# Kernel optimization log

Hardware: AMD Instinct MI355X
Metric: run time of the kernel (lower is better)

## Reference

```python
import jax, jax.numpy as jnp
import numpy as np

N = 50000
E = 800000
IN_C = 64
OUT_C = 64
EPS = 1 + 1e-06


def setup_inputs() -> dict:
    key = jax.random.key(0)
    ks = jax.random.split(key, 10)
    x = jax.random.normal(ks[0], (N, IN_C), dtype=jnp.float32)
    lower_indices = jax.random.randint(ks[1], (2, E), 0, N, dtype=jnp.int64)
    lower_values = jax.random.uniform(ks[2], (E,), dtype=jnp.float32)
    upper_indices = jax.random.randint(ks[3], (2, E), 0, N, dtype=jnp.int64)
    upper_values = jax.random.uniform(ks[4], (E,), dtype=jnp.float32)
    s = 1.0 / np.sqrt(IN_C)
    w_lower = jax.random.uniform(ks[5], (IN_C, OUT_C), jnp.float32, -s, s)
    a_lower = jax.random.uniform(ks[6], (2 * OUT_C,), jnp.float32, -s, s)
    w_upper = jax.random.uniform(ks[7], (IN_C, OUT_C), jnp.float32, -s, s)
    a_upper = jax.random.uniform(ks[8], (2 * OUT_C,), jnp.float32, -s, s)
    w_lin = jax.random.uniform(ks[9], (IN_C, OUT_C), jnp.float32, -s, s)
    return {
        "x": x,
        "lower_indices": lower_indices,
        "lower_values": lower_values,
        "upper_indices": upper_indices,
        "upper_values": upper_values,
        "w_lower": w_lower,
        "a_lower": a_lower,
        "w_upper": w_upper,
        "a_upper": a_upper,
        "w_lin": w_lin,
    }


def _att_conv(x, weight, att_w, indices, values):
    """TopoModelX base Conv with att=True.

    x_msg = x @ weight; per edge (i=target, j=source):
      alpha_e = elu(concat(x_msg[j], x_msg[i]) @ att_w) * nbhd_vals_e
    out[i] = sum_e alpha_e * x_msg[j]
    """
    xm = x @ weight                              # [N, out]
    i, j = indices[0], indices[1]                # target, source
    # concat(src, tgt) @ a == src @ a[:F] + tgt @ a[F:]; precompute per-node
    s_src = xm @ att_w[:OUT_C]                   # [N]
    s_tgt = xm @ att_w[OUT_C:]                   # [N]
    alpha = jax.nn.elu(s_src[j] + s_tgt[i]) * values   # [E]
    msg = alpha[:, None] * xm[j]                 # [E, out]
    return jax.ops.segment_sum(msg, i, num_segments=N)


def reference(x, lower_indices, lower_values, upper_indices, upper_values,
              w_lower, a_lower, w_upper, a_upper, w_lin):
    lower_x = _att_conv(x, w_lower, a_lower, lower_indices, lower_values)
    upper_x = _att_conv(x, w_upper, a_upper, upper_indices, upper_values)
    w_x = (x @ w_lin) * EPS
    # Aggregation(aggr_func='sum', update_func='relu')
    return jax.nn.relu(lower_x + upper_x + w_x)
```

## Files before the change

### kernel.cpp

```cpp
#include <hip/hip_runtime.h>
#include <hip/hip_bf16.h>
#include <math.h>

#define N_NODES 50000
#define N_EDGES 800000
#define C 64
#define EPS_F 1.000001f

#define CAPN 48
#define NCNT (2 * N_NODES)
#define OVF_IDX NCNT
#define OMAX 4096

#define RB_BITS 7
#define RBUK (1 << RB_BITS)
#define NREG ((NCNT + RBUK - 1) >> RB_BITS)
#define RCAP 2560
#define EPB 8192
#define NP1 ((2 * N_EDGES + EPB - 1) / EPB)
#define NPREB 784
#define NK1 (NP1 + NPREB)

#define ZERON (NCNT + 1 + NREG)

#define RANGE 16
#define NGATH (N_NODES / RANGE)
#define LDS_STRIDE 66

#define NPRE ((N_NODES + 31) / 32)

typedef __attribute__((ext_vector_type(8))) unsigned short u16x8;

__device__ __forceinline__ unsigned short f2bf(float f) {
    unsigned u = __float_as_uint(f);
    return (unsigned short)((u + 0x7FFFu + ((u >> 16) & 1u)) >> 16);
}
__device__ __forceinline__ float bf2f(unsigned short b) {
    return __uint_as_float(((unsigned)b) << 16);
}

__global__ __launch_bounds__(256) void s_kernel(
    const float* __restrict__ x,
    const float* __restrict__ w_l, const float* __restrict__ a_l,
    const float* __restrict__ w_u, const float* __restrict__ a_u,
    float* __restrict__ ssl, float* __restrict__ stl,
    float* __restrict__ ssu, float* __restrict__ stu,
    int* __restrict__ cnt)
{
    const int b = blockIdx.x;
    const int t = threadIdx.x;

    const int gz = b * 256 + t;
    if (gz < ZERON) cnt[gz] = 0;

    __shared__ float wa[4 * C];
    {
        const int v = t >> 6;
        const int k = t & 63;
        const float* __restrict__ w = (v < 2) ? w_l : w_u;
        const float* __restrict__ a = (v < 2) ? a_l : a_u;
        const int ao = (v & 1) * C;
        float acc = 0.f;
#pragma unroll 16
        for (int o = 0; o < C; ++o)
            acc = fmaf(w[k * C + o], a[ao + o], acc);
        wa[v * C + k] = acc;
    }
    __syncthreads();

    const int lane = t & 63;
    const int wv = t >> 6;
    const int row0 = b * 32 + wv * 8;
    if (row0 >= N_NODES) return;

    const float wls = wa[lane], wlt = wa[C + lane];
    const float wus = wa[2 * C + lane], wut = wa[3 * C + lane];

#pragma unroll
    for (int r = 0; r < 8; ++r) {
        const int row = row0 + r;
        if (row >= N_NODES) break;
        const float xv = x[row * C + lane];
        float psl = xv * wls, ptl = xv * wlt;
        float psu = xv * wus, ptu = xv * wut;
#pragma unroll
        for (int o = 32; o >= 1; o >>= 1) {
            psl += __shfl_xor(psl, o);
            ptl += __shfl_xor(ptl, o);
            psu += __shfl_xor(psu, o);
            ptu += __shfl_xor(ptu, o);
        }
        if (lane == 0) {
            ssl[row] = psl; stl[row] = ptl;
            ssu[row] = psu; stu[row] = ptu;
        }
    }
}

__global__ __launch_bounds__(512) void gemm_scatter_kernel(
    const float* __restrict__ x,
    const float* __restrict__ w_l, const float* __restrict__ w_u,
    const float* __restrict__ w_lin,
    const int* __restrict__ lidx, const float* __restrict__ lval,
    const int* __restrict__ uidx, const float* __restrict__ uval,
    const float* __restrict__ ssl, const float* __restrict__ stl,
    const float* __restrict__ ssu, const float* __restrict__ stu,
    unsigned short* __restrict__ xm_l, unsigned short* __restrict__ xm_u,
    float* __restrict__ xlin,
    int* __restrict__ cnt, uint2* __restrict__ rbuf, int2* __restrict__ ovf)
{
    const int b = blockIdx.x, t = threadIdx.x;
    __shared__ int hist[NREG];

    if (b % 5 == 0) {
        const int p = b / 5;
        int* __restrict__ rcur = cnt + NCNT + 1;

        for (int s0 = t; s0 < NREG; s0 += 512) hist[s0] = 0;
        __syncthreads();

        unsigned lo[16];
        int bk[16];
        const int gbase = p * EPB + t;
#pragma unroll
        for (int k = 0; k < 16; ++k) {
            const int g = gbase + k * 512;
            bk[k] = -1;
            if (g < 2 * N_EDGES) {
                int i, j;
                float v, s;
                if (g < N_EDGES) {
                    i = lidx[g]; j = lidx[N_EDGES + g]; v = lval[g];
                    s = ssl[j] + stl[i];
                    bk[k] = i;
                } else {
                    const int e = g - N_EDGES;
                    i = uidx[e]; j = uidx[N_EDGES + e]; v = uval[e];
                    s = ssu[j] + stu[i];
                    bk[k] = N_NODES + i;
                }
                s = (s > 0.f) ? s : expm1f(s);
                lo[k] = ((unsigned)j << 16) | (unsigned)f2bf(s * v);
                atomicAdd(&hist[bk[k] >> RB_BITS], 1);
            }
        }
        __syncthreads();

        for (int cb = t; cb < NREG; cb += 512) {
            const int c = hist[cb];
            hist[cb] = c ? atomicAdd(&rcur[cb], c) : 0;
        }
        __syncthreads();

#pragma unroll
        for (int k = 0; k < 16; ++k) {
            if (bk[k] >= 0) {
                const int cb = bk[k] >> RB_BITS;
                const int slot = atomicAdd(&hist[cb], 1);
                if (slot < RCAP) {
                    rbuf[(size_t)cb * RCAP + slot] = make_uint2(lo[k], (unsigned)bk[k]);
                } else {
                    const int oi = atomicAdd(&cnt[OVF_IDX], 1);
                    if (oi < OMAX) ovf[oi] = make_int2(bk[k], (int)lo[k]);
                }
            }
        }
        return;
    }

    const int pid = b - b / 5 - 1;
    const int lane = t & 63;
    const int wvu = __builtin_amdgcn_readfirstlane(t >> 6);
    const int row0 = pid * 64 + wvu * 8;
    if (row0 >= N_NODES) return;

    const float* xr[8];
#pragma unroll
    for (int r = 0; r < 8; ++r) {
        int rr = row0 + r;
        if (rr >= N_NODES) rr = N_NODES - 1;
        xr[r] = x + (size_t)rr * C;
    }

    float acc_l[8] = {0,0,0,0,0,0,0,0};
    float acc_u[8] = {0,0,0,0,0,0,0,0};
    float acc_n[8] = {0,0,0,0,0,0,0,0};

#pragma unroll 1
    for (int kc = 0; kc < C; kc += 4) {
#pragma unroll
        for (int kk = 0; kk < 4; ++kk) {
            const int k = kc + kk;
            const float wl = w_l[k * C + lane];
            const float wu = w_u[k * C + lane];
            const float wn = w_lin[k * C + lane];
#pragma unroll
            for (int r = 0; r < 8; ++r) {
                const float xk = xr[r][k];
                acc_l[r] = fmaf(xk, wl, acc_l[r]);
                acc_u[r] = fmaf(xk, wu, acc_u[r]);
                acc_n[r] = fmaf(xk, wn, acc_n[r]);
            }
        }
    }

#pragma unroll
    for (int r = 0; r < 8; ++r) {
        const int row = row0 + r;
        if (row < N_NODES) {
            xm_l[row * C + lane] = f2bf(acc_l[r]);
            xm_u[row * C + lane] = f2bf(acc_u[r]);
            xlin[row * C + lane] = acc_n[r] * EPS_F;
        }
    }
}

__global__ __launch_bounds__(256) void distrib_kernel(
    int* __restrict__ cnt, const uint2* __restrict__ rbuf,
    unsigned* __restrict__ rec, int2* __restrict__ ovf)
{
    const int cb = blockIdx.x, t = threadIdx.x;
    __shared__ int cur[RBUK];
    if (t < RBUK) cur[t] = 0;
    __syncthreads();

    const int* __restrict__ rcur = cnt + NCNT + 1;
    const int n = min(rcur[cb], RCAP);
    const uint2* __restrict__ rb = rbuf + (size_t)cb * RCAP;

    for (int r = t; r < n; r += 256) {
        const uint2 e = rb[r];
        const int local = (int)e.y & (RBUK - 1);
        const int rank = atomicAdd(&cur[local], 1);
        if (rank < CAPN) {
            rec[(size_t)e.y * CAPN + rank] = e.x;
        } else {
            const int oi = atomicAdd(&cnt[OVF_IDX], 1);
            if (oi < OMAX) ovf[oi] = make_int2((int)e.y, (int)e.x);
        }
    }
    __syncthreads();

    if (t < RBUK) {
        const int bucket = (cb << RB_BITS) + t;
        if (bucket < NCNT) cnt[bucket] = cur[t];
    }
}

__global__ __launch_bounds__(256) void gather_kernel(
    const float* __restrict__ xlin,
    const int* __restrict__ cnt, const unsigned* __restrict__ rec,
    const int2* __restrict__ ovf,
    const unsigned short* __restrict__ xm_l, const unsigned short* __restrict__ xm_u,
    float* __restrict__ out)
{
    const int r = blockIdx.x;
    const int t = threadIdx.x;
    const int wv = t >> 6, lane = t & 63;
    const int sub8 = lane >> 3;
    const int cg = lane & 7;

    __shared__ float racc[RANGE * LDS_STRIDE];

    const int oc = min(cnt[OVF_IDX], OMAX);

#pragma unroll 1
    for (int nsel = 0; nsel < 4; ++nsel) {
        const int node = r * RANGE + wv * 4 + nsel;
        const int bA = node;
        const int bB = N_NODES + node;
        const int lenA = min(cnt[bA], CAPN);
        const int lenB = min(cnt[bB], CAPN);
        const unsigned* __restrict__ rbA = rec + (size_t)bA * CAPN;
        const unsigned* __restrict__ rbB = rec + (size_t)bB * CAPN;

        float acc[8] = {0.f,0.f,0.f,0.f,0.f,0.f,0.f,0.f};
        int kA = 0, kB = 0;
        while ((kA < lenA) | (kB < lenB)) {
            const int iA = kA + sub8, iB = kB + sub8;
            const bool aA = iA < lenA, aB = iB < lenB;
            const unsigned rwA = rbA[aA ? iA : kA];
            const unsigned rwB = rbB[aB ? iB : kB];
            const int jA = aA ? (int)(rwA >> 16) : 0;
            const int jB = aB ? (int)(rwB >> 16) : 0;
            const float wA = aA ? bf2f((unsigned short)(rwA & 0xFFFFu)) : 0.f;
            const float wB = aB ? bf2f((unsigned short)(rwB & 0xFFFFu)) : 0.f;
            const u16x8 rowA = *(const u16x8*)(xm_l + jA * C + cg * 8);
            const u16x8 rowB = *(const u16x8*)(xm_u + jB * C + cg * 8);
#pragma unroll
            for (int c = 0; c < 8; ++c)
                acc[c] = fmaf(wA, bf2f(rowA[c]), acc[c]);
#pragma unroll
            for (int c = 0; c < 8; ++c)
                acc[c] = fmaf(wB, bf2f(rowB[c]), acc[c]);
            kA += (kA < lenA) ? 8 : 0;
            kB += (kB < lenB) ? 8 : 0;
        }

        for (int u = 0; u < oc; ++u) {
            const int2 e = ovf[u];
            if (e.x == bA || e.x == bB) {
                const unsigned rw = (unsigned)e.y;
                const int j = (int)(rw >> 16);
                const float w = (sub8 == 0) ? bf2f((unsigned short)(rw & 0xFFFFu)) : 0.f;
                const unsigned short* xm = (e.x == bA) ? xm_l : xm_u;
                const u16x8 row = *(const u16x8*)(xm + j * C + cg * 8);
#pragma unroll
                for (int c = 0; c < 8; ++c)
                    acc[c] = fmaf(w, bf2f(row[c]), acc[c]);
            }
        }

#pragma unroll
        for (int o = 8; o <= 32; o <<= 1)
#pragma unroll
            for (int c = 0; c < 8; ++c)
                acc[c] += __shfl_xor(acc[c], o);
        const int nl = wv * 4 + nsel;
        if (lane < 8) {
#pragma unroll
            for (int c = 0; c < 8; ++c)
                racc[nl * LDS_STRIDE + lane * 8 + c] = acc[c];
        }
    }
    __syncthreads();

    const int base_node = r * RANGE;
#pragma unroll
    for (int rep = 0; rep < 4; ++rep) {
        const int flat = rep * 256 + t;
        const int nl = flat >> 6, ch = flat & 63;
        const int node = base_node + nl;
        const float v = racc[nl * LDS_STRIDE + ch] + xlin[node * C + ch];
        out[node * C + ch] = fmaxf(v, 0.f);
    }
}

extern "C" void kernel_launch(void* const* d_in, const int* in_sizes, int n_in,
                              void* d_out, int out_size, void* d_ws, size_t ws_size,
                              hipStream_t stream)
{
    const float* x          = (const float*)d_in[0];
    const int*   lower_idx  = (const int*)d_in[1];
    const float* lower_vals = (const float*)d_in[2];
    const int*   upper_idx  = (const int*)d_in[3];
    const float* upper_vals = (const float*)d_in[4];
    const float* w_lower    = (const float*)d_in[5];
    const float* a_lower    = (const float*)d_in[6];
    const float* w_upper    = (const float*)d_in[7];
    const float* a_upper    = (const float*)d_in[8];
    const float* w_lin      = (const float*)d_in[9];

    float* out = (float*)d_out;
    char* ws = (char*)d_ws;

    const size_t NC_F = (size_t)N_NODES * C * sizeof(float);
    const size_t NC_H = (size_t)N_NODES * C * sizeof(unsigned short);
    unsigned short* xm_l = (unsigned short*)ws;  ws += NC_H;
    unsigned short* xm_u = (unsigned short*)ws;  ws += NC_H;
    float* xlin = (float*)ws;                 ws += NC_F;
    float* ssl  = (float*)ws;                 ws += N_NODES * sizeof(float);
    float* stl  = (float*)ws;                 ws += N_NODES * sizeof(float);
    float* ssu  = (float*)ws;                 ws += N_NODES * sizeof(float);
    float* stu  = (float*)ws;                 ws += N_NODES * sizeof(float);
    int2* ovf   = (int2*)ws;                  ws += OMAX * sizeof(int2);
    uint2* rbuf = (uint2*)ws;                 ws += (size_t)NREG * RCAP * sizeof(uint2);
    int* cnt    = (int*)ws;                   ws += (size_t)(ZERON + 32) * sizeof(int);
    unsigned* rec = (unsigned*)ws;            ws += ((size_t)NCNT * CAPN + 64) * sizeof(unsigned);

    s_kernel<<<NPRE, 256, 0, stream>>>(
        x, w_lower, a_lower, w_upper, a_upper,
        ssl, stl, ssu, stu, cnt);

    gemm_scatter_kernel<<<NK1, 512, 0, stream>>>(
        x, w_lower, w_upper, w_lin,
        lower_idx, lower_vals, upper_idx, upper_vals,
        ssl, stl, ssu, stu,
        xm_l, xm_u, xlin, cnt, rbuf, ovf);

    distrib_kernel<<<NREG, 256, 0, stream>>>(cnt, rbuf, rec, ovf);

    gather_kernel<<<NGATH, 256, 0, stream>>>(
        xlin, cnt, rec, ovf, xm_l, xm_u, out);
}
```

Measured before the change: 200.2 us.

## Fuse bucket distribution into gather using LDS lists and interleaved buckets

Bucket IDs are interleaved (2*i for lower, 2*i+1 for upper) so that each coarse region of 128 buckets covers 64 nodes. The distrib kernel is removed. The gather kernel now builds per-node edge lists in shared memory straight from the region buffer and then aggregates, which drops the global rec array write and read plus one kernel launch. Per-block overflow goes to a small LDS list. The new block uses about 25KB of LDS and 512 threads, which may lower occupancy.

```diff
diff --git a/kernel.cpp b/kernel.cpp
--- a/kernel.cpp
+++ b/kernel.cpp
@@ -8,24 +8,21 @@
 #define EPS_F 1.000001f
 
 #define CAPN 48
-#define NCNT (2 * N_NODES)
-#define OVF_IDX NCNT
+#define OVF_IDX 0
 #define OMAX 4096
+#define LOVF 64
 
 #define RB_BITS 7
 #define RBUK (1 << RB_BITS)
-#define NREG ((NCNT + RBUK - 1) >> RB_BITS)
+#define NBUCK (2 * N_NODES)
+#define NREG ((NBUCK + RBUK - 1) >> RB_BITS)
 #define RCAP 2560
 #define EPB 8192
 #define NP1 ((2 * N_EDGES + EPB - 1) / EPB)
 #define NPREB 784
 #define NK1 (NP1 + NPREB)
 
-#define ZERON (NCNT + 1 + NREG)
-
-#define RANGE 16
-#define NGATH (N_NODES / RANGE)
-#define LDS_STRIDE 66
+#define ZERON (1 + NREG)
 
 #define NPRE ((N_NODES + 31) / 32)
 
@@ -114,7 +111,7 @@
 
     if (b % 5 == 0) {
         const int p = b / 5;
-        int* __restrict__ rcur = cnt + NCNT + 1;
+        int* __restrict__ rcur = cnt + 1;
 
         for (int s0 = t; s0 < NREG; s0 += 512) hist[s0] = 0;
         __syncthreads();
@@ -132,12 +129,12 @@
                 if (g < N_EDGES) {
                     i = lidx[g]; j = lidx[N_EDGES + g]; v = lval[g];
                     s = ssl[j] + stl[i];
-                    bk[k] = i;
+                    bk[k] = 2 * i;
                 } else {
                     const int e = g - N_EDGES;
                     i = uidx[e]; j = uidx[N_EDGES + e]; v = uval[e];
                     s = ssu[j] + stu[i];
-                    bk[k] = N_NODES + i;
+                    bk[k] = 2 * i + 1;
                 }
                 s = (s > 0.f) ? s : expm1f(s);
                 lo[k] = ((unsigned)j << 16) | (unsigned)f2bf(s * v);
@@ -215,72 +212,65 @@
     }
 }
 
-__global__ __launch_bounds__(256) void distrib_kernel(
-    int* __restrict__ cnt, const uint2* __restrict__ rbuf,
-    unsigned* __restrict__ rec, int2* __restrict__ ovf)
+__global__ __launch_bounds__(512) void gather_kernel(
+    const float* __restrict__ xlin,
+    const int* __restrict__ cnt, const uint2* __restrict__ rbuf,
+    const int2* __restrict__ ovf,
+    const unsigned short* __restrict__ xm_l, const unsigned short* __restrict__ xm_u,
+    float* __restrict__ out)
 {
-    const int cb = blockIdx.x, t = threadIdx.x;
+    const int cb = blockIdx.x;
+    const int t = threadIdx.x;
+    const int wv = t >> 6, lane = t & 63;
+    const int sub8 = lane >> 3;
+    const int cg = lane & 7;
+
+    __shared__ unsigned lists[RBUK * CAPN];
     __shared__ int cur[RBUK];
-    if (t < RBUK) cur[t] = 0;
+    __shared__ int lovf_bk[LOVF];
+    __shared__ unsigned lovf_rc[LOVF];
+    __shared__ int lc;
+
+    for (int s0 = t; s0 < RBUK; s0 += 512) cur[s0] = 0;
+    if (t == 0) lc = 0;
     __syncthreads();
 
-    const int* __restrict__ rcur = cnt + NCNT + 1;
-    const int n = min(rcur[cb], RCAP);
+    const int n = min(cnt[1 + cb], RCAP);
     const uint2* __restrict__ rb = rbuf + (size_t)cb * RCAP;
-
-    for (int r = t; r < n; r += 256) {
+    for (int r = t; r < n; r += 512) {
         const uint2 e = rb[r];
         const int local = (int)e.y & (RBUK - 1);
         const int rank = atomicAdd(&cur[local], 1);
         if (rank < CAPN) {
-            rec[(size_t)e.y * CAPN + rank] = e.x;
+            lists[local * CAPN + rank] = e.x;
         } else {
-            const int oi = atomicAdd(&cnt[OVF_IDX], 1);
-            if (oi < OMAX) ovf[oi] = make_int2((int)e.y, (int)e.x);
+            const int o = atomicAdd(&lc, 1);
+            if (o < LOVF) { lovf_bk[o] = local; lovf_rc[o] = e.x; }
         }
     }
     __syncthreads();
 
-    if (t < RBUK) {
-        const int bucket = (cb << RB_BITS) + t;
-        if (bucket < NCNT) cnt[bucket] = cur[t];
-    }
-}
-
-__global__ __launch_bounds__(256) void gather_kernel(
-    const float* __restrict__ xlin,
-    const int* __restrict__ cnt, const unsigned* __restrict__ rec,
-    const int2* __restrict__ ovf,
-    const unsigned short* __restrict__ xm_l, const unsigned short* __restrict__ xm_u,
-    float* __restrict__ out)
-{
-    const int r = blockIdx.x;
-    const int t = threadIdx.x;
-    const int wv = t >> 6, lane = t & 63;
-    const int sub8 = lane >> 3;
-    const int cg = lane & 7;
-
-    __shared__ float racc[RANGE * LDS_STRIDE];
-
     const int oc = min(cnt[OVF_IDX], OMAX);
+    const int lc2 = min(lc, LOVF);
 
 #pragma unroll 1
-    for (int nsel = 0; nsel < 4; ++nsel) {
-        const int node = r * RANGE + wv * 4 + nsel;
-        const int bA = node;
-        const int bB = N_NODES + node;
-        const int lenA = min(cnt[bA], CAPN);
-        const int lenB = min(cnt[bB], CAPN);
-        const unsigned* __restrict__ rbA = rec + (size_t)bA * CAPN;
-        const unsigned* __restrict__ rbB = rec + (size_t)bB * CAPN;
+    for (int p = 0; p < 8; ++p) {
+        const int q = wv * 8 + p;
+        const int node = cb * 64 + q;
+        if (node >= N_NODES) break;
+        const int lA = 2 * q, lB = 2 * q + 1;
+        const int lenA = min(cur[lA], CAPN);
+        const int lenB = min(cur[lB], CAPN);
+        const unsigned* __restrict__ lstA = lists + lA * CAPN;
+        const unsigned* __restrict__ lstB = lists + lB * CAPN;
 
         float acc[8] = {0.f,0.f,0.f,0.f,0.f,0.f,0.f,0.f};
         int kA = 0, kB = 0;
         while ((kA < lenA) | (kB < lenB)) {
             const int iA = kA + sub8, iB = kB + sub8;
             const bool aA = iA < lenA, aB = iB < lenB;
-            const unsigned rwA = rbA[aA ? iA : kA];
-            const unsigned rwB = rbB[aB ? iB : kB];
+            const unsigned rwA = lstA[aA ? iA : kA];
+            const unsigned rwB = lstB[aB ? iB : kB];
             const int jA = aA ? (int)(rwA >> 16) : 0;
             const int jB = aB ? (int)(rwB >> 16) : 0;
             const float wA = aA ? bf2f((unsigned short)(rwA & 0xFFFFu)) : 0.f;
@@ -299,11 +289,11 @@
 
         for (int u = 0; u < oc; ++u) {
             const int2 e = ovf[u];
-            if (e.x == bA || e.x == bB) {
+            if (e.x == 2 * node || e.x == 2 * node + 1) {
                 const unsigned rw = (unsigned)e.y;
                 const int j = (int)(rw >> 16);
                 const float w = (sub8 == 0) ? bf2f((unsigned short)(rw & 0xFFFFu)) : 0.f;
-                const unsigned short* xm = (e.x == bA) ? xm_l : xm_u;
+                const unsigned short* xm = (e.x & 1) ? xm_u : xm_l;
                 const u16x8 row = *(const u16x8*)(xm + j * C + cg * 8);
 #pragma unroll
                 for (int c = 0; c < 8; ++c)
@@ -311,28 +301,43 @@
             }
         }
 
+        for (int u = 0; u < lc2; ++u) {
+            const int bkl = lovf_bk[u];
+            if (bkl == lA || bkl == lB) {
+                const unsigned rw = lovf_rc[u];
+                const int j = (int)(rw >> 16);
+                const float w = (sub8 == 0) ? bf2f((unsigned short)(rw & 0xFFFFu)) : 0.f;
+                const unsigned short* xm = (bkl & 1) ? xm_u : xm_l;
+                const u16x8 row = *(const u16x8*)(xm + j * C + cg * 8);
+#pragma unroll
+                for (int c = 0; c < 8; ++c)
+                    acc[c] = fmaf(w, bf2f(row[c]), acc[c]);
+            }
+        }
+
 #pragma unroll
         for (int o = 8; o <= 32; o <<= 1)
 #pragma unroll
             for (int c = 0; c < 8; ++c)
                 acc[c] += __shfl_xor(acc[c], o);
-        const int nl = wv * 4 + nsel;
+
         if (lane < 8) {
-#pragma unroll
-            for (int c = 0; c < 8; ++c)
-                racc[nl * LDS_STRIDE + lane * 8 + c] = acc[c];
-        }
-    }
-    __syncthreads();
-
-    const int base_node = r * RANGE;
-#pragma unroll
-    for (int rep = 0; rep < 4; ++rep) {
-        const int flat = rep * 256 + t;
-        const int nl = flat >> 6, ch = flat & 63;
-        const int node = base_node + nl;
-        const float v = racc[nl * LDS_STRIDE + ch] + xlin[node * C + ch];
-        out[node * C + ch] = fmaxf(v, 0.f);
+            const float* __restrict__ xl = xlin + (size_t)node * C + lane * 8;
+            const float4 xa = *(const float4*)(xl);
+            const float4 xb = *(const float4*)(xl + 4);
+            float4 oa, ob;
+            oa.x = fmaxf(acc[0] + xa.x, 0.f);
+            oa.y = fmaxf(acc[1] + xa.y, 0.f);
+            oa.z = fmaxf(acc[2] + xa.z, 0.f);
+            oa.w = fmaxf(acc[3] + xa.w, 0.f);
+            ob.x = fmaxf(acc[4] + xb.x, 0.f);
+            ob.y = fmaxf(acc[5] + xb.y, 0.f);
+            ob.z = fmaxf(acc[6] + xb.z, 0.f);
+            ob.w = fmaxf(acc[7] + xb.w, 0.f);
+            float* __restrict__ op = out + (size_t)node * C + lane * 8;
+            *(float4*)(op) = oa;
+            *(float4*)(op + 4) = ob;
+        }
     }
 }
 
@@ -366,7 +371,6 @@
     int2* ovf   = (int2*)ws;                  ws += OMAX * sizeof(int2);
     uint2* rbuf = (uint2*)ws;                 ws += (size_t)NREG * RCAP * sizeof(uint2);
     int* cnt    = (int*)ws;                   ws += (size_t)(ZERON + 32) * sizeof(int);
-    unsigned* rec = (unsigned*)ws;            ws += ((size_t)NCNT * CAPN + 64) * sizeof(unsigned);
 
     s_kernel<<<NPRE, 256, 0, stream>>>(
         x, w_lower, a_lower, w_upper, a_upper,
@@ -378,8 +382,6 @@
         ssl, stl, ssu, stu,
         xm_l, xm_u, xlin, cnt, rbuf, ovf);
 
-    distrib_kernel<<<NREG, 256, 0, stream>>>(cnt, rbuf, rec, ovf);
-
-    gather_kernel<<<NGATH, 256, 0, stream>>>(
-        xlin, cnt, rec, ovf, xm_l, xm_u, out);
-}
+    gather_kernel<<<NREG, 512, 0, stream>>>(
+        xlin, cnt, rbuf, ovf, xm_l, xm_u, out);
+}
```

Measured after the change: 193.1 us. -3.5%, faster.
